# Optimization experiments

Measured on AMD Instinct MI355X. Metric: run time of the kernel, lower is better.

The kernel has to match this reference:

```python
import jax, jax.numpy as jnp
import numpy as np

B, C, H, W = 4, 32, 32, 1024
PATCH = 21           # patch_size in spatial_correlation_sample
DIL = 2              # dilation_patch
PAD = DIL * (PATCH - 1) // 2  # 20: max displacement, zero-padded out-of-range samples


def setup_inputs() -> dict:
    key = jax.random.key(0)
    k1, k2 = jax.random.split(key)
    x1 = jax.random.normal(k1, (B, C, H, W), dtype=jnp.float32)
    x2 = jax.random.normal(k2, (B, C, H, W), dtype=jnp.float32)
    return {"x1": x1, "x2": x2}


def _correlate(x1, x2):
    # spatial_correlation_sample(kernel_size=1, patch_size=21, stride=1,
    #                            padding=0, dilation_patch=2)
    # out[b, pi, pj, h, w] = sum_c x1[b,c,h,w] * x2[b,c,h+2*(pi-10), w+2*(pj-10)]
    # with out-of-bounds x2 samples treated as zero.
    b, c, h, w = x1.shape
    x2p = jnp.pad(x2, ((0, 0), (0, 0), (PAD, PAD), (PAD, PAD)))
    chans = []
    for i in range(PATCH):      # fixed 21x21 displacement grid (static slices)
        for j in range(PATCH):
            win = jax.lax.slice(x2p, (0, 0, DIL * i, DIL * j),
                                (b, c, DIL * i + h, DIL * j + w))
            chans.append(jnp.einsum('bchw,bchw->bhw', x1, win))
    corr = jnp.stack(chans, axis=1) / c  # (b, 441, h, w), normalized by n_channels
    return jax.nn.leaky_relu(corr, negative_slope=0.1)


def reference(x1, x2):
    # CorrelationNetwork.forward returns only out_correlation; the conv/deconv
    # flow pyramid does not contribute to the returned tensor (and the
    # visualize_flow calls reference undefined symbols in the original).
    return _correlate(x1, x2)
```

## Files before the change

### kernel.cpp

```cpp
#include <hip/hip_runtime.h>
#include <stdint.h>

#define BB     4
#define CC     32
#define HH     32
#define WW     1024
#define PATCH  21
#define RAD    10
#define PADW   20
#define CHUNKC 2
#define NP     (CC / CHUNKC)
#define NGR    266
#define ROWF   (NGR * 4)
#define BUFF   (CHUNKC * ROWF)
#define CSTR   (HH * WW)

typedef __attribute__((address_space(3))) uint32_t lds_u32_t;
typedef __attribute__((address_space(1))) const uint32_t glb_u32_t;

__device__ __forceinline__ int swz(int s) { return s ^ ((s >> 3) & 1); }

__device__ __forceinline__ void stage_dma(const float* __restrict__ src0,
                                          float* __restrict__ sbuf, int tid) {
#pragma unroll
    for (int t = 0; t < 3; t++) {
        const int idx = tid + t * 256;
        if (idx < CHUNKC * NGR) {
            const int c  = (idx >= NGR) ? 1 : 0;
            const int q  = idx - c * NGR;
            const int gq = swz(q);
            const int base_gran = (tid & ~63) + t * 256;
            lds_u32_t* dst = (lds_u32_t*)(sbuf + base_gran * 4);
            const float* src = src0 + (size_t)c * CSTR + (gq * 4 - PADW);
            if (gq >= 5 && gq <= 260)
                __builtin_amdgcn_global_load_lds((glb_u32_t*)src, dst, 16, 0, 0);
        }
    }
}

__global__ __launch_bounds__(256, 5)
void corr_kernel(const float* __restrict__ x1, const float* __restrict__ x2,
                 float* __restrict__ out) {
    __shared__ float sx2[2 * BUFF + 16];

    const int tid = threadIdx.x;
    const int tw  = tid & 127;
    const int th2 = tid >> 7;

    const int lid    = blockIdx.x;
    const int xcd    = lid & 7;
    const int t8     = lid >> 3;
    const int sharer = t8 % 48;
    const int rowd   = t8 / 48;
    const int row    = rowd * 8 + xcd;
    const int r2i    = row >> 2;
    const int b      = row & 3;
    const int s      = sharer & 7;
    const int z      = sharer >> 3;
    const int r2     = r2i - PADW;

    const int pi_hi = min(20, (r2 + 20) >> 1);
    const int pi_lo = max(0, (r2 - 10) >> 1);
    const int L     = pi_hi - pi_lo + 1;
    const int e0    = 2 * s;
    if (e0 >= L) return;

    const int  pi0  = pi_hi - e0;
    const int  h0   = r2 + 20 - 2 * pi0;
    const bool has1 = (e0 + 1) < L;
    const int  pi1  = pi0 - 1;
    const int  h1   = h0 + 2;

    const int  pjb    = 4 * z + 2 * th2;
    const bool st0    = (pjb     <= 20);
    const bool st1    = (pjb + 1 <= 20);
    const bool active = st0;
    const int  w8     = tw * 8;

    float* out0 = out + (((size_t)(b * PATCH * PATCH + pi0 * PATCH + pjb)) * HH + h0) * WW + w8;
    float* out1 = out + (((size_t)(b * PATCH * PATCH + pi1 * PATCH + pjb)) * HH + h1) * WW + w8;

    if ((unsigned)r2 >= (unsigned)HH) {
        float4 zv = make_float4(0.f, 0.f, 0.f, 0.f);
        if (active) {
#pragma unroll
            for (int j = 0; j < 2; j++) {
                if (j == 0 ? st0 : st1) {
                    *(float4*)(out0 + (size_t)j * CSTR)     = zv;
                    *(float4*)(out0 + (size_t)j * CSTR + 4) = zv;
                    if (has1) {
                        *(float4*)(out1 + (size_t)j * CSTR)     = zv;
                        *(float4*)(out1 + (size_t)j * CSTR + 4) = zv;
                    }
                }
            }
        }
        return;
    }

    if (tid < 40) {
        const int rr = tid / 10, g = tid % 10;
        const int slot = (g < 5) ? g : (256 + g);
        *(float4*)(sx2 + rr * ROWF + 4 * slot) = make_float4(0.f, 0.f, 0.f, 0.f);
    }

    const int g0 = active ? (2 * tw + 2 * z + th2) : (2 * tw);
    int ps0 = 4 * swz(g0), ps1 = 4 * swz(g0 + 1), ps2 = 4 * swz(g0 + 2);

    const float* x2base = x2 + ((size_t)(b * CC) * HH + r2) * WW;
    const float* x1p0   = x1 + ((size_t)(b * CC) * HH + h0) * WW + w8;
    const float* x1p1   = has1 ? (x1p0 + 2 * WW) : x1p0;

    stage_dma(x2base, sx2, tid);
    __syncthreads();

    float acc0[2][8], acc1[2][8];
#pragma unroll
    for (int j = 0; j < 2; j++)
#pragma unroll
        for (int k = 0; k < 8; k++) { acc0[j][k] = 0.f; acc1[j][k] = 0.f; }

    for (int p = 0; p < NP; p++) {
        if (p + 1 < NP)
            stage_dma(x2base + (size_t)(p + 1) * CHUNKC * CSTR,
                      sx2 + ((p + 1) & 1) * BUFF, tid);
        if (active) {
            const float* buf = sx2 + (p & 1) * BUFF;
#pragma unroll
            for (int c = 0; c < CHUNKC; c++) {
                const float* row_p = buf + c * ROWF;
                float win[12];
                *(float4*)&win[0] = *(const float4*)(row_p + ps0);
                *(float4*)&win[4] = *(const float4*)(row_p + ps1);
                *(float4*)&win[8] = *(const float4*)(row_p + ps2);

                const float* xa = x1p0 + (size_t)(CHUNKC * p + c) * CSTR;
                const float* xb = x1p1 + (size_t)(CHUNKC * p + c) * CSTR;
                float4 a00 = *(const float4*)xa, a01 = *(const float4*)(xa + 4);
                float4 a10 = *(const float4*)xb, a11 = *(const float4*)(xb + 4);
                const float a0[8] = {a00.x, a00.y, a00.z, a00.w, a01.x, a01.y, a01.z, a01.w};
                const float a1[8] = {a10.x, a10.y, a10.z, a10.w, a11.x, a11.y, a11.z, a11.w};

#pragma unroll
                for (int j = 0; j < 2; j++)
#pragma unroll
                    for (int k = 0; k < 8; k++) {
                        const float wv = win[k + 2 * j];
                        acc0[j][k] = fmaf(a0[k], wv, acc0[j][k]);
                        acc1[j][k] = fmaf(a1[k], wv, acc1[j][k]);
                    }
            }
        }
        if (p + 1 < NP) __syncthreads();
    }

    if (!active) return;

    const float inv_c = 1.0f / (float)CC;
#pragma unroll
    for (int j = 0; j < 2; j++) {
        if (j == 0 ? st0 : st1) {
            float4 o0, o1, q0, q1;
            float* po0 = (float*)&o0; float* po1 = (float*)&o1;
            float* pq0 = (float*)&q0; float* pq1 = (float*)&q1;
#pragma unroll
            for (int k = 0; k < 4; k++) {
                float v0 = acc0[j][k]     * inv_c;
                float v1 = acc0[j][4 + k] * inv_c;
                float u0 = acc1[j][k]     * inv_c;
                float u1 = acc1[j][4 + k] * inv_c;
                po0[k] = v0 > 0.f ? v0 : 0.1f * v0;
                po1[k] = v1 > 0.f ? v1 : 0.1f * v1;
                pq0[k] = u0 > 0.f ? u0 : 0.1f * u0;
                pq1[k] = u1 > 0.f ? u1 : 0.1f * u1;
            }
            *(float4*)(out0 + (size_t)j * CSTR)     = o0;
            *(float4*)(out0 + (size_t)j * CSTR + 4) = o1;
            if (has1) {
                *(float4*)(out1 + (size_t)j * CSTR)     = q0;
                *(float4*)(out1 + (size_t)j * CSTR + 4) = q1;
            }
        }
    }
}

extern "C" void kernel_launch(void* const* d_in, const int* in_sizes, int n_in,
                              void* d_out, int out_size, void* d_ws, size_t ws_size,
                              hipStream_t stream) {
    const float* x1 = (const float*)d_in[0];
    const float* x2 = (const float*)d_in[1];
    float* out = (float*)d_out;

    dim3 grid(72 * 4 * 8 * 6, 1, 1);
    dim3 block(256, 1, 1);
    corr_kernel<<<grid, block, 0, stream>>>(x1, x2, out);
}
```

Baseline: 359.5 us.

## Replace LDS-staged x2 rows with direct per-thread global float4 loads

Removes the double-buffered LDS staging of x2 through global_load_lds DMA, along with its per-chunk barriers. Each thread now loads its three x2 float4 windows straight from global memory, with bounds predicates that substitute zeros at the edges. This drops the synchronization and LDS traffic and lets idle threads exit early. The cost is redundant global and L2 reads, since neighbouring threads and blocks re-read overlapping x2 data that was previously shared through LDS.

New measurement: 1.090 ms. 203% more time.

```diff
diff --git a/kernel.cpp b/kernel.cpp
--- a/kernel.cpp
+++ b/kernel.cpp
@@ -8,41 +8,11 @@
 #define PATCH  21
 #define RAD    10
 #define PADW   20
-#define CHUNKC 2
-#define NP     (CC / CHUNKC)
-#define NGR    266
-#define ROWF   (NGR * 4)
-#define BUFF   (CHUNKC * ROWF)
 #define CSTR   (HH * WW)
-
-typedef __attribute__((address_space(3))) uint32_t lds_u32_t;
-typedef __attribute__((address_space(1))) const uint32_t glb_u32_t;
-
-__device__ __forceinline__ int swz(int s) { return s ^ ((s >> 3) & 1); }
-
-__device__ __forceinline__ void stage_dma(const float* __restrict__ src0,
-                                          float* __restrict__ sbuf, int tid) {
-#pragma unroll
-    for (int t = 0; t < 3; t++) {
-        const int idx = tid + t * 256;
-        if (idx < CHUNKC * NGR) {
-            const int c  = (idx >= NGR) ? 1 : 0;
-            const int q  = idx - c * NGR;
-            const int gq = swz(q);
-            const int base_gran = (tid & ~63) + t * 256;
-            lds_u32_t* dst = (lds_u32_t*)(sbuf + base_gran * 4);
-            const float* src = src0 + (size_t)c * CSTR + (gq * 4 - PADW);
-            if (gq >= 5 && gq <= 260)
-                __builtin_amdgcn_global_load_lds((glb_u32_t*)src, dst, 16, 0, 0);
-        }
-    }
-}
 
 __global__ __launch_bounds__(256, 5)
 void corr_kernel(const float* __restrict__ x1, const float* __restrict__ x2,
                  float* __restrict__ out) {
-    __shared__ float sx2[2 * BUFF + 16];
-
     const int tid = threadIdx.x;
     const int tw  = tid & 127;
     const int th2 = tid >> 7;
@@ -71,48 +41,38 @@
     const int  pi1  = pi0 - 1;
     const int  h1   = h0 + 2;
 
-    const int  pjb    = 4 * z + 2 * th2;
-    const bool st0    = (pjb     <= 20);
-    const bool st1    = (pjb + 1 <= 20);
-    const bool active = st0;
-    const int  w8     = tw * 8;
+    const int pjb = 4 * z + 2 * th2;
+    if (pjb > 20) return;
+    const bool st1 = (pjb + 1 <= 20);
+    const int  w8  = tw * 8;
 
     float* out0 = out + (((size_t)(b * PATCH * PATCH + pi0 * PATCH + pjb)) * HH + h0) * WW + w8;
     float* out1 = out + (((size_t)(b * PATCH * PATCH + pi1 * PATCH + pjb)) * HH + h1) * WW + w8;
 
     if ((unsigned)r2 >= (unsigned)HH) {
         float4 zv = make_float4(0.f, 0.f, 0.f, 0.f);
-        if (active) {
 #pragma unroll
-            for (int j = 0; j < 2; j++) {
-                if (j == 0 ? st0 : st1) {
-                    *(float4*)(out0 + (size_t)j * CSTR)     = zv;
-                    *(float4*)(out0 + (size_t)j * CSTR + 4) = zv;
-                    if (has1) {
-                        *(float4*)(out1 + (size_t)j * CSTR)     = zv;
-                        *(float4*)(out1 + (size_t)j * CSTR + 4) = zv;
-                    }
+        for (int j = 0; j < 2; j++) {
+            if (j == 0 || st1) {
+                *(float4*)(out0 + (size_t)j * CSTR)     = zv;
+                *(float4*)(out0 + (size_t)j * CSTR + 4) = zv;
+                if (has1) {
+                    *(float4*)(out1 + (size_t)j * CSTR)     = zv;
+                    *(float4*)(out1 + (size_t)j * CSTR + 4) = zv;
                 }
             }
         }
         return;
     }
 
-    if (tid < 40) {
-        const int rr = tid / 10, g = tid % 10;
-        const int slot = (g < 5) ? g : (256 + g);
-        *(float4*)(sx2 + rr * ROWF + 4 * slot) = make_float4(0.f, 0.f, 0.f, 0.f);
-    }
+    const int  u0 = w8 + 2 * pjb - PADW;
+    const bool v0 = (u0     >= 0) && (u0     <= WW - 4);
+    const bool v1 = (u0 + 4 >= 0) && (u0 + 4 <= WW - 4);
+    const bool v2 = (u0 + 8 >= 0) && (u0 + 8 <= WW - 4);
 
-    const int g0 = active ? (2 * tw + 2 * z + th2) : (2 * tw);
-    int ps0 = 4 * swz(g0), ps1 = 4 * swz(g0 + 1), ps2 = 4 * swz(g0 + 2);
-
-    const float* x2base = x2 + ((size_t)(b * CC) * HH + r2) * WW;
-    const float* x1p0   = x1 + ((size_t)(b * CC) * HH + h0) * WW + w8;
-    const float* x1p1   = has1 ? (x1p0 + 2 * WW) : x1p0;
-
-    stage_dma(x2base, sx2, tid);
-    __syncthreads();
+    const float* x2p = x2 + ((size_t)(b * CC) * HH + r2) * WW + u0;
+    const float* xap = x1 + ((size_t)(b * CC) * HH + h0) * WW + w8;
+    const float* xbp = has1 ? (xap + 2 * WW) : xap;
 
     float acc0[2][8], acc1[2][8];
 #pragma unroll
@@ -120,59 +80,49 @@
 #pragma unroll
         for (int k = 0; k < 8; k++) { acc0[j][k] = 0.f; acc1[j][k] = 0.f; }
 
-    for (int p = 0; p < NP; p++) {
-        if (p + 1 < NP)
-            stage_dma(x2base + (size_t)(p + 1) * CHUNKC * CSTR,
-                      sx2 + ((p + 1) & 1) * BUFF, tid);
-        if (active) {
-            const float* buf = sx2 + (p & 1) * BUFF;
-#pragma unroll
-            for (int c = 0; c < CHUNKC; c++) {
-                const float* row_p = buf + c * ROWF;
-                float win[12];
-                *(float4*)&win[0] = *(const float4*)(row_p + ps0);
-                *(float4*)&win[4] = *(const float4*)(row_p + ps1);
-                *(float4*)&win[8] = *(const float4*)(row_p + ps2);
+    const float4 zv4 = make_float4(0.f, 0.f, 0.f, 0.f);
+    for (int c = 0; c < CC; ++c) {
+        float4 wv0 = v0 ? *(const float4*)(x2p)     : zv4;
+        float4 wv1 = v1 ? *(const float4*)(x2p + 4) : zv4;
+        float4 wv2 = v2 ? *(const float4*)(x2p + 8) : zv4;
+        float win[12] = {wv0.x, wv0.y, wv0.z, wv0.w,
+                         wv1.x, wv1.y, wv1.z, wv1.w,
+                         wv2.x, wv2.y, wv2.z, wv2.w};
 
-                const float* xa = x1p0 + (size_t)(CHUNKC * p + c) * CSTR;
-                const float* xb = x1p1 + (size_t)(CHUNKC * p + c) * CSTR;
-                float4 a00 = *(const float4*)xa, a01 = *(const float4*)(xa + 4);
-                float4 a10 = *(const float4*)xb, a11 = *(const float4*)(xb + 4);
-                const float a0[8] = {a00.x, a00.y, a00.z, a00.w, a01.x, a01.y, a01.z, a01.w};
-                const float a1[8] = {a10.x, a10.y, a10.z, a10.w, a11.x, a11.y, a11.z, a11.w};
+        float4 a00 = *(const float4*)xap, a01 = *(const float4*)(xap + 4);
+        float4 a10 = *(const float4*)xbp, a11 = *(const float4*)(xbp + 4);
+        const float a0[8] = {a00.x, a00.y, a00.z, a00.w, a01.x, a01.y, a01.z, a01.w};
+        const float a1[8] = {a10.x, a10.y, a10.z, a10.w, a11.x, a11.y, a11.z, a11.w};
 
 #pragma unroll
-                for (int j = 0; j < 2; j++)
+        for (int j = 0; j < 2; j++)
 #pragma unroll
-                    for (int k = 0; k < 8; k++) {
-                        const float wv = win[k + 2 * j];
-                        acc0[j][k] = fmaf(a0[k], wv, acc0[j][k]);
-                        acc1[j][k] = fmaf(a1[k], wv, acc1[j][k]);
-                    }
+            for (int k = 0; k < 8; k++) {
+                const float wv = win[k + 2 * j];
+                acc0[j][k] = fmaf(a0[k], wv, acc0[j][k]);
+                acc1[j][k] = fmaf(a1[k], wv, acc1[j][k]);
             }
-        }
-        if (p + 1 < NP) __syncthreads();
+
+        x2p += CSTR; xap += CSTR; xbp += CSTR;
     }
-
-    if (!active) return;
 
     const float inv_c = 1.0f / (float)CC;
 #pragma unroll
     for (int j = 0; j < 2; j++) {
-        if (j == 0 ? st0 : st1) {
+        if (j == 0 || st1) {
             float4 o0, o1, q0, q1;
             float* po0 = (float*)&o0; float* po1 = (float*)&o1;
             float* pq0 = (float*)&q0; float* pq1 = (float*)&q1;
 #pragma unroll
             for (int k = 0; k < 4; k++) {
-                float v0 = acc0[j][k]     * inv_c;
-                float v1 = acc0[j][4 + k] * inv_c;
-                float u0 = acc1[j][k]     * inv_c;
-                float u1 = acc1[j][4 + k] * inv_c;
-                po0[k] = v0 > 0.f ? v0 : 0.1f * v0;
-                po1[k] = v1 > 0.f ? v1 : 0.1f * v1;
-                pq0[k] = u0 > 0.f ? u0 : 0.1f * u0;
-                pq1[k] = u1 > 0.f ? u1 : 0.1f * u1;
+                float v0o = acc0[j][k]     * inv_c;
+                float v1o = acc0[j][4 + k] * inv_c;
+                float u0o = acc1[j][k]     * inv_c;
+                float u1o = acc1[j][4 + k] * inv_c;
+                po0[k] = v0o > 0.f ? v0o : 0.1f * v0o;
+                po1[k] = v1o > 0.f ? v1o : 0.1f * v1o;
+                pq0[k] = u0o > 0.f ? u0o : 0.1f * u0o;
+                pq1[k] = u1o > 0.f ? u1o : 0.1f * u1o;
             }
             *(float4*)(out0 + (size_t)j * CSTR)     = o0;
             *(float4*)(out0 + (size_t)j * CSTR + 4) = o1;
```
